# Optimization experiments

Hardware: AMD Instinct MI355X
Metric: run time of the kernel (lower is better)

Reference implementation:

```python
import jax, jax.numpy as jnp
import numpy as np

D_IN, H1, H2, B, K = 128, 128, 64, 262144, 4

def _mk(key, shape):
    return jax.random.normal(key, shape, dtype=jnp.float32) * 0.05

def setup_inputs() -> dict:
    key = jax.random.key(0)
    ks = jax.random.split(key, 40)
    inp = {
        'x': jax.random.normal(ks[0], (B, 96), dtype=jnp.float32),
        'u': jax.random.normal(ks[1], (B, 32), dtype=jnp.float32),
        'mix_factor': jax.random.uniform(ks[2], (1,), dtype=jnp.float32),
        'teacher_P': jax.random.uniform(ks[3], (K,), dtype=jnp.float32),
    }
    # main critic params (torch Linear: W [out,in], b [out])
    dims = [(H1, D_IN), (H1, H1), (H2, H1), (1, H2)] * 2  # l1..l4, l5..l8
    for i, (o, ii) in enumerate(dims):
        inp[f'W{i+1}'] = _mk(ks[4 + 2 * i], (o, ii))
        inp[f'b{i+1}'] = _mk(ks[5 + 2 * i], (o,))
    # stacked teacher params (K teachers), only l1,l2,l3,l5,l6,l7 are used
    tdims = {'1': (H1, D_IN), '2': (H1, H1), '3': (H2, H1), '5': (H1, D_IN), '6': (H1, H1), '7': (H2, H1)}
    j = 20
    for name, (o, ii) in tdims.items():
        inp[f'tW{name}'] = _mk(ks[j], (K, o, ii)); j += 1
        inp[f'tb{name}'] = _mk(ks[j], (K, o)); j += 1
    return inp

def reference(x, u, mix_factor, teacher_P, W1, b1, W2, b2, W3, b3, W4, b4, W5, b5, W6, b6, W7, b7, W8, b8, tW1, tb1, tW2, tb2, tW3, tb3, tW5, tb5, tW6, tb6, tW7, tb7):
    m = mix_factor  # [1], broadcasts
    P = teacher_P   # [K]
    xu = jnp.concatenate([x, u], axis=1)  # [B, 128]

    lin = lambda h, W, b: h @ W.T + b
    # teacher linear on shared input [B,I] -> [K,B,O]
    tlin0 = lambda h, W, b: jnp.einsum('bi,koi->kbo', h, W) + b[:, None, :]
    # teacher linear on per-teacher streams [K,B,I] -> [K,B,O]
    tlin = lambda h, W, b: jnp.einsum('kbi,koi->kbo', h, W) + b[:, None, :]
    mixsum = lambda ht: jnp.einsum('kbo,k->bo', ht, P)

    def head(W_a, b_a, W_b, b_b, W_c, b_c, W_d, b_d, tWa, tba, tWb, tbb, tWc, tbc):
        ht = tlin0(xu, tWa, tba)                                   # [K,B,128]
        h = jax.nn.relu(lin(xu, W_a, b_a) * (1 - m) + mixsum(ht) * m)
        ht = jax.nn.relu(ht)
        ht2 = tlin(ht, tWb, tbb)
        h = jax.nn.relu(lin(h, W_b, b_b) * (1 - m) + mixsum(ht2) * m)
        ht2 = jax.nn.relu(ht2)
        ht3 = tlin(ht2, tWc, tbc)
        h = jax.nn.relu(lin(h, W_c, b_c) * (1 - m) + mixsum(ht3) * m)
        return lin(h, W_d, b_d)                                    # [B,1]

    x1 = head(W1, b1, W2, b2, W3, b3, W4, b4, tW1, tb1, tW2, tb2, tW3, tb3)
    x2 = head(W5, b5, W6, b6, W7, b7, W8, b8, tW5, tb5, tW6, tb6, tW7, tb7)
    return (x1, x2)
```

## Files before the change

### kernel.cpp

```cpp
#include <hip/hip_runtime.h>
#include <hip/hip_bf16.h>
#include <stdint.h>

#define B_TOTAL 262144
#define TB 64
#define SLOT 16384
#define BUF1 81920
#define LDS_BYTES 163840
#define HEAD_W 204800

typedef short v8s __attribute__((ext_vector_type(8)));
typedef float v4f __attribute__((ext_vector_type(4)));

union Frag { uint4 q; uint32_t d[4]; v8s v; };

__device__ __forceinline__ uint32_t pack2(float a, float b) {
    union { __hip_bfloat162 h; uint32_t u; } p;
    p.h = __float22bfloat162_rn(make_float2(a, b));
    return p.u;
}


struct KParams {
    const float* x; const float* u; const float* mix; const float* P;
    const float* mb[6];
    const float* tb[6];
    const float* Wout[2];
    const float* bout[2];
    const unsigned short* wbf;
    float* out;
};

struct PrepParams { const float* src[12]; unsigned short* dst; };

__global__ __launch_bounds__(256) void prep_kernel(PrepParams pp) {
    const int ends[12] = {16384,81920,98304,163840,172032,204800,
                          221184,286720,303104,368640,376832,409600};
    int gi = (blockIdx.x * 256 + threadIdx.x) * 4;
    if (gi >= 409600) return;
    int s = 0;
    #pragma unroll
    for (int i = 0; i < 12; ++i) { if (gi >= ends[i]) s = i + 1; }
    int base = (s == 0) ? 0 : ends[s - 1];
    const float4 f = *(const float4*)(pp.src[s] + (gi - base));
    *(uint2*)(pp.dst + gi) = make_uint2(pack2(f.x, f.y), pack2(f.z, f.w));
}

__device__ __forceinline__ void stage_xu(char* lds, const float* x, const float* u,
                                         int rowBase, int tid)
{
    for (int G = tid; G < 1024; G += 512) {
        const int row = G >> 4;
        const int gg  = G & 15;
        const int grow = rowBase + row;
        float4 fa, fb;
        if (gg < 12) {
            const float* s2 = x + grow * 96 + gg * 8;
            fa = *(const float4*)s2; fb = *(const float4*)(s2 + 4);
        } else {
            const float* s2 = u + grow * 32 + (gg - 12) * 8;
            fa = *(const float4*)s2; fb = *(const float4*)(s2 + 4);
        }
        *(uint4*)(lds + row * 256 + ((gg ^ (row & 15)) << 4)) =
            make_uint4(pack2(fa.x, fa.y), pack2(fa.z, fa.w),
                       pack2(fb.x, fb.y), pack2(fb.z, fb.w));
    }
}

template<bool SHARED_IN, int N>
__device__ __forceinline__ void layer_fwd(char* lds, int inOff, int outOff,
        const unsigned short* W, const float* mbias, const float* tbias,
        float c0, const float* cP, int lane, int wave,
        const float* Wout, float* pgrid)
{
    constexpr bool FINAL = (N == 64);
    constexpr int NBT = FINAL ? 2 : 4;
    const int l15  = lane & 15;
    const int quad = lane >> 4;
    const int colBase = FINAL ? ((wave >> 1) << 4) : (wave << 4);
    const int btBase  = FINAL ? ((wave & 1) << 1) : 0;

    v4f acc[5][NBT];
    #pragma unroll
    for (int s = 0; s < 5; ++s)
        #pragma unroll
        for (int bt = 0; bt < NBT; ++bt)
            acc[s][bt] = (v4f){0.f, 0.f, 0.f, 0.f};

    const unsigned short* wRow = W + (colBase + l15) * 128 + quad * 8;

    #pragma unroll
    for (int ks = 0; ks < 4; ++ks) {
        Frag xS[NBT];
        const int gg = ks * 4 + quad;
        if constexpr (SHARED_IN) {
            #pragma unroll
            for (int bt = 0; bt < NBT; ++bt) {
                const int row = (btBase + bt) * 16 + l15;
                xS[bt].q = *(const uint4*)(lds + inOff + row * 256 + ((gg ^ (row & 15)) << 4));
            }
        }
        #pragma unroll
        for (int s = 0; s < 5; ++s) {
            Frag xF[NBT];
            if constexpr (!SHARED_IN) {
                #pragma unroll
                for (int bt = 0; bt < NBT; ++bt) {
                    const int row = (btBase + bt) * 16 + l15;
                    xF[bt].q = *(const uint4*)(lds + inOff + s * SLOT + row * 256
                                               + ((gg ^ (row & 15)) << 4));
                }
            }
            Frag wF;
            wF.q = *(const uint4*)(wRow + s * (N * 128) + ks * 32);
            #pragma unroll
            for (int bt = 0; bt < NBT; ++bt)
                acc[s][bt] = __builtin_amdgcn_mfma_f32_16x16x32_bf16(
                    wF.v, (SHARED_IN ? xS[bt].v : xF[bt].v), acc[s][bt], 0, 0, 0);
        }
    }

    const int obase = colBase + quad * 4;
    const float4 mB = *(const float4*)(mbias + obase);
    float4 tB[4];
    #pragma unroll
    for (int s = 0; s < 4; ++s)
        tB[s] = *(const float4*)(tbias + s * N + obase);

    if constexpr (!FINAL) {
        #pragma unroll
        for (int bt = 0; bt < 4; ++bt) {
            const int row = bt * 16 + l15;
            char* ab = lds + outOff + row * 256 + (((obase >> 3) ^ (row & 15)) << 4)
                       + ((obase & 7) << 1);
            float vr[4];
            vr[0] = c0 * (acc[0][bt][0] + mB.x);
            vr[1] = c0 * (acc[0][bt][1] + mB.y);
            vr[2] = c0 * (acc[0][bt][2] + mB.z);
            vr[3] = c0 * (acc[0][bt][3] + mB.w);
            uint2 tw[4];
            #pragma unroll
            for (int s = 0; s < 4; ++s) {
                float t0 = acc[s + 1][bt][0] + tB[s].x;
                float t1 = acc[s + 1][bt][1] + tB[s].y;
                float t2 = acc[s + 1][bt][2] + tB[s].z;
                float t3 = acc[s + 1][bt][3] + tB[s].w;
                vr[0] = fmaf(cP[s], t0, vr[0]);
                vr[1] = fmaf(cP[s], t1, vr[1]);
                vr[2] = fmaf(cP[s], t2, vr[2]);
                vr[3] = fmaf(cP[s], t3, vr[3]);
                tw[s] = make_uint2(pack2(fmaxf(t0, 0.f), fmaxf(t1, 0.f)),
                                   pack2(fmaxf(t2, 0.f), fmaxf(t3, 0.f)));
            }
            *(uint2*)ab = make_uint2(pack2(fmaxf(vr[0], 0.f), fmaxf(vr[1], 0.f)),
                                     pack2(fmaxf(vr[2], 0.f), fmaxf(vr[3], 0.f)));
            #pragma unroll
            for (int s = 0; s < 4; ++s)
                *(uint2*)(ab + (s + 1) * SLOT) = tw[s];
        }
    } else {
        const float4 wo = *(const float4*)(Wout + obase);
        float psum[NBT];
        #pragma unroll
        for (int j = 0; j < NBT; ++j) {
            float vr[4];
            vr[0] = c0 * (acc[0][j][0] + mB.x);
            vr[1] = c0 * (acc[0][j][1] + mB.y);
            vr[2] = c0 * (acc[0][j][2] + mB.z);
            vr[3] = c0 * (acc[0][j][3] + mB.w);
            #pragma unroll
            for (int s = 0; s < 4; ++s) {
                vr[0] = fmaf(cP[s], acc[s + 1][j][0] + tB[s].x, vr[0]);
                vr[1] = fmaf(cP[s], acc[s + 1][j][1] + tB[s].y, vr[1]);
                vr[2] = fmaf(cP[s], acc[s + 1][j][2] + tB[s].z, vr[2]);
                vr[3] = fmaf(cP[s], acc[s + 1][j][3] + tB[s].w, vr[3]);
            }
            float pp = fmaxf(vr[0], 0.f) * wo.x + fmaxf(vr[1], 0.f) * wo.y
                     + fmaxf(vr[2], 0.f) * wo.z + fmaxf(vr[3], 0.f) * wo.w;
            pp += __shfl_xor(pp, 16);
            pp += __shfl_xor(pp, 32);
            psum[j] = pp;
        }
        if (lane < 16) {
            #pragma unroll
            for (int j = 0; j < NBT; ++j)
                pgrid[(wave >> 1) * 64 + (btBase + j) * 16 + lane] = psum[j];
        }
    }
}

extern "C" __global__ __launch_bounds__(512, 2)
void critic_kernel(KParams p)
{
    extern __shared__ char lds[];
    const int tid  = threadIdx.x;
    const int lane = tid & 63;
    const int wave = tid >> 6;
    const int rowBase = blockIdx.x * TB;

    const float m  = p.mix[0];
    const float c0 = 1.f - m;
    float cP[4];
    #pragma unroll
    for (int k = 0; k < 4; ++k) cP[k] = m * p.P[k];

    stage_xu(lds, p.x, p.u, rowBase, tid);

    #pragma unroll 1
    for (int head = 0; head < 2; ++head) {
        __syncthreads();
        const unsigned short* wb = p.wbf + head * HEAD_W;
        const int hb = head * 3;

        layer_fwd<true, 128>(lds, 0, BUF1, wb, p.mb[hb + 0], p.tb[hb + 0],
                             c0, cP, lane, wave, nullptr, nullptr);
        __syncthreads();
        layer_fwd<false, 128>(lds, BUF1, 0, wb + 81920, p.mb[hb + 1], p.tb[hb + 1],
                              c0, cP, lane, wave, nullptr, nullptr);
        __syncthreads();
        layer_fwd<false, 64>(lds, 0, 0, wb + 163840, p.mb[hb + 2], p.tb[hb + 2],
                             c0, cP, lane, wave, p.Wout[head], (float*)(lds + BUF1));
        __syncthreads();

        if (tid < 64) {
            const float* pg = (const float*)(lds + BUF1);
            p.out[head * B_TOTAL + rowBase + tid] =
                p.bout[head][0] + pg[tid] + pg[64 + tid] + pg[128 + tid] + pg[192 + tid];
        }
        if (head == 0)
            stage_xu(lds, p.x, p.u, rowBase, tid);
    }
}

extern "C" void kernel_launch(void* const* d_in, const int* in_sizes, int n_in,
                              void* d_out, int out_size, void* d_ws, size_t ws_size,
                              hipStream_t stream)
{
    (void)in_sizes; (void)n_in; (void)out_size; (void)ws_size;

    PrepParams pp;
    const int sidx[12] = {4, 20, 6, 22, 8, 24, 12, 26, 14, 28, 16, 30};
    for (int i = 0; i < 12; ++i) pp.src[i] = (const float*)d_in[sidx[i]];
    pp.dst = (unsigned short*)d_ws;

    KParams kp;
    kp.x = (const float*)d_in[0];  kp.u = (const float*)d_in[1];
    kp.mix = (const float*)d_in[2]; kp.P = (const float*)d_in[3];
    const int mbi[6] = {5, 7, 9, 13, 15, 17};
    const int tbi[6] = {21, 23, 25, 27, 29, 31};
    for (int i = 0; i < 6; ++i) {
        kp.mb[i] = (const float*)d_in[mbi[i]];
        kp.tb[i] = (const float*)d_in[tbi[i]];
    }
    kp.Wout[0] = (const float*)d_in[10]; kp.Wout[1] = (const float*)d_in[18];
    kp.bout[0] = (const float*)d_in[11]; kp.bout[1] = (const float*)d_in[19];
    kp.wbf = (const unsigned short*)d_ws;
    kp.out = (float*)d_out;

    (void)hipFuncSetAttribute((const void*)critic_kernel,
                              hipFuncAttributeMaxDynamicSharedMemorySize, LDS_BYTES);

    hipLaunchKernelGGL(prep_kernel, dim3(400), dim3(256), 0, stream, pp);
    hipLaunchKernelGGL(critic_kernel, dim3(4096), dim3(512), LDS_BYTES, stream, kp);
}
```

Baseline: 883.2 us.

## Halve batch tile, raise occupancy, and prefetch double-buffered weight fragments

```diff
diff --git a/kernel.cpp b/kernel.cpp
--- a/kernel.cpp
+++ b/kernel.cpp
@@ -3,10 +3,10 @@
 #include <stdint.h>
 
 #define B_TOTAL 262144
-#define TB 64
-#define SLOT 16384
-#define BUF1 81920
-#define LDS_BYTES 163840
+#define TB 32
+#define SLOT 8192
+#define BUF1 40960
+#define LDS_BYTES 81920
 #define HEAD_W 204800
 
 typedef short v8s __attribute__((ext_vector_type(8)));
@@ -49,36 +49,52 @@
 __device__ __forceinline__ void stage_xu(char* lds, const float* x, const float* u,
                                          int rowBase, int tid)
 {
-    for (int G = tid; G < 1024; G += 512) {
-        const int row = G >> 4;
-        const int gg  = G & 15;
-        const int grow = rowBase + row;
-        float4 fa, fb;
-        if (gg < 12) {
-            const float* s2 = x + grow * 96 + gg * 8;
-            fa = *(const float4*)s2; fb = *(const float4*)(s2 + 4);
-        } else {
-            const float* s2 = u + grow * 32 + (gg - 12) * 8;
-            fa = *(const float4*)s2; fb = *(const float4*)(s2 + 4);
-        }
-        *(uint4*)(lds + row * 256 + ((gg ^ (row & 15)) << 4)) =
-            make_uint4(pack2(fa.x, fa.y), pack2(fa.z, fa.w),
-                       pack2(fb.x, fb.y), pack2(fb.z, fb.w));
-    }
+    const int row = tid >> 4;
+    const int gg  = tid & 15;
+    const int grow = rowBase + row;
+    float4 fa, fb;
+    if (gg < 12) {
+        const float* s2 = x + grow * 96 + gg * 8;
+        fa = *(const float4*)s2; fb = *(const float4*)(s2 + 4);
+    } else {
+        const float* s2 = u + grow * 32 + (gg - 12) * 8;
+        fa = *(const float4*)s2; fb = *(const float4*)(s2 + 4);
+    }
+    *(uint4*)(lds + row * 256 + ((gg ^ (row & 15)) << 4)) =
+        make_uint4(pack2(fa.x, fa.y), pack2(fa.z, fa.w),
+                   pack2(fb.x, fb.y), pack2(fb.z, fb.w));
+}
+
+struct WPre0 { Frag w0[4]; };
+
+template<int N>
+__device__ __forceinline__ WPre0 preload0(const unsigned short* W, int lane, int wave)
+{
+    WPre0 r;
+    const int l15  = lane & 15;
+    const int quad = lane >> 4;
+    const int colBase = (N == 64) ? ((wave >> 1) << 4) : (wave << 4);
+    const unsigned short* wRow = W + (colBase + l15) * 128 + quad * 8;
+    #pragma unroll
+    for (int ks = 0; ks < 4; ++ks)
+        r.w0[ks].q = *(const uint4*)(wRow + ks * 32);
+    return r;
 }
 
 template<bool SHARED_IN, int N>
-__device__ __forceinline__ void layer_fwd(char* lds, int inOff, int outOff,
-        const unsigned short* W, const float* mbias, const float* tbias,
+__device__ __forceinline__ void compute(char* lds, int inOff, int outOff,
+        const WPre0& wp, const unsigned short* W,
+        const float* mbias, const float* tbias,
         float c0, const float* cP, int lane, int wave,
         const float* Wout, float* pgrid)
 {
     constexpr bool FINAL = (N == 64);
-    constexpr int NBT = FINAL ? 2 : 4;
+    constexpr int NBT = FINAL ? 1 : 2;
     const int l15  = lane & 15;
     const int quad = lane >> 4;
     const int colBase = FINAL ? ((wave >> 1) << 4) : (wave << 4);
-    const int btBase  = FINAL ? ((wave & 1) << 1) : 0;
+    const int btBase  = FINAL ? (wave & 1) : 0;
+    const unsigned short* wRow = W + (colBase + l15) * 128 + quad * 8;
 
     v4f acc[5][NBT];
     #pragma unroll
@@ -87,36 +103,50 @@
         for (int bt = 0; bt < NBT; ++bt)
             acc[s][bt] = (v4f){0.f, 0.f, 0.f, 0.f};
 
-    const unsigned short* wRow = W + (colBase + l15) * 128 + quad * 8;
-
-    #pragma unroll
-    for (int ks = 0; ks < 4; ++ks) {
-        Frag xS[NBT];
-        const int gg = ks * 4 + quad;
-        if constexpr (SHARED_IN) {
+    Frag wf[2][4];
+    #pragma unroll
+    for (int ks = 0; ks < 4; ++ks) wf[0][ks] = wp.w0[ks];
+
+    Frag xS[4 * NBT];
+    if constexpr (SHARED_IN) {
+        #pragma unroll
+        for (int ks = 0; ks < 4; ++ks) {
+            const int gg = ks * 4 + quad;
             #pragma unroll
             for (int bt = 0; bt < NBT; ++bt) {
                 const int row = (btBase + bt) * 16 + l15;
-                xS[bt].q = *(const uint4*)(lds + inOff + row * 256 + ((gg ^ (row & 15)) << 4));
+                xS[ks * NBT + bt].q =
+                    *(const uint4*)(lds + inOff + row * 256 + ((gg ^ (row & 15)) << 4));
             }
         }
-        #pragma unroll
-        for (int s = 0; s < 5; ++s) {
-            Frag xF[NBT];
+    }
+
+    #pragma unroll
+    for (int s = 0; s < 5; ++s) {
+        if (s < 4) {
+            #pragma unroll
+            for (int ks = 0; ks < 4; ++ks)
+                wf[(s + 1) & 1][ks].q =
+                    *(const uint4*)(wRow + (s + 1) * (N * 128) + ks * 32);
+        }
+        #pragma unroll
+        for (int ks = 0; ks < 4; ++ks) {
+            const int gg = ks * 4 + quad;
+            Frag xf[NBT];
             if constexpr (!SHARED_IN) {
                 #pragma unroll
                 for (int bt = 0; bt < NBT; ++bt) {
                     const int row = (btBase + bt) * 16 + l15;
-                    xF[bt].q = *(const uint4*)(lds + inOff + s * SLOT + row * 256
+                    xf[bt].q = *(const uint4*)(lds + inOff + s * SLOT + row * 256
                                                + ((gg ^ (row & 15)) << 4));
                 }
             }
-            Frag wF;
-            wF.q = *(const uint4*)(wRow + s * (N * 128) + ks * 32);
             #pragma unroll
             for (int bt = 0; bt < NBT; ++bt)
                 acc[s][bt] = __builtin_amdgcn_mfma_f32_16x16x32_bf16(
-                    wF.v, (SHARED_IN ? xS[bt].v : xF[bt].v), acc[s][bt], 0, 0, 0);
+                    wf[s & 1][ks].v,
+                    (SHARED_IN ? xS[ks * NBT + bt].v : xf[bt].v),
+                    acc[s][bt], 0, 0, 0);
         }
     }
 
@@ -129,8 +159,8 @@
 
     if constexpr (!FINAL) {
         #pragma unroll
-        for (int bt = 0; bt < 4; ++bt) {
-            const int row = bt * 16 + l15;
+        for (int bt = 0; bt < NBT; ++bt) {
+            const int row = (btBase + bt) * 16 + l15;
             char* ab = lds + outOff + row * 256 + (((obase >> 3) ^ (row & 15)) << 4)
                        + ((obase & 7) << 1);
             float vr[4];
@@ -160,36 +190,28 @@
         }
     } else {
         const float4 wo = *(const float4*)(Wout + obase);
-        float psum[NBT];
-        #pragma unroll
-        for (int j = 0; j < NBT; ++j) {
-            float vr[4];
-            vr[0] = c0 * (acc[0][j][0] + mB.x);
-            vr[1] = c0 * (acc[0][j][1] + mB.y);
-            vr[2] = c0 * (acc[0][j][2] + mB.z);
-            vr[3] = c0 * (acc[0][j][3] + mB.w);
-            #pragma unroll
-            for (int s = 0; s < 4; ++s) {
-                vr[0] = fmaf(cP[s], acc[s + 1][j][0] + tB[s].x, vr[0]);
-                vr[1] = fmaf(cP[s], acc[s + 1][j][1] + tB[s].y, vr[1]);
-                vr[2] = fmaf(cP[s], acc[s + 1][j][2] + tB[s].z, vr[2]);
-                vr[3] = fmaf(cP[s], acc[s + 1][j][3] + tB[s].w, vr[3]);
-            }
-            float pp = fmaxf(vr[0], 0.f) * wo.x + fmaxf(vr[1], 0.f) * wo.y
-                     + fmaxf(vr[2], 0.f) * wo.z + fmaxf(vr[3], 0.f) * wo.w;
-            pp += __shfl_xor(pp, 16);
-            pp += __shfl_xor(pp, 32);
-            psum[j] = pp;
-        }
-        if (lane < 16) {
-            #pragma unroll
-            for (int j = 0; j < NBT; ++j)
-                pgrid[(wave >> 1) * 64 + (btBase + j) * 16 + lane] = psum[j];
-        }
-    }
-}
-
-extern "C" __global__ __launch_bounds__(512, 2)
+        float vr[4];
+        vr[0] = c0 * (acc[0][0][0] + mB.x);
+        vr[1] = c0 * (acc[0][0][1] + mB.y);
+        vr[2] = c0 * (acc[0][0][2] + mB.z);
+        vr[3] = c0 * (acc[0][0][3] + mB.w);
+        #pragma unroll
+        for (int s = 0; s < 4; ++s) {
+            vr[0] = fmaf(cP[s], acc[s + 1][0][0] + tB[s].x, vr[0]);
+            vr[1] = fmaf(cP[s], acc[s + 1][0][1] + tB[s].y, vr[1]);
+            vr[2] = fmaf(cP[s], acc[s + 1][0][2] + tB[s].z, vr[2]);
+            vr[3] = fmaf(cP[s], acc[s + 1][0][3] + tB[s].w, vr[3]);
+        }
+        float pp = fmaxf(vr[0], 0.f) * wo.x + fmaxf(vr[1], 0.f) * wo.y
+                 + fmaxf(vr[2], 0.f) * wo.z + fmaxf(vr[3], 0.f) * wo.w;
+        pp += __shfl_xor(pp, 16);
+        pp += __shfl_xor(pp, 32);
+        if (lane < 16)
+            pgrid[(wave >> 1) * 32 + btBase * 16 + lane] = pp;
+    }
+}
+
+extern "C" __global__ __launch_bounds__(512, 4)
 void critic_kernel(KParams p)
 {
     extern __shared__ char lds[];
@@ -208,24 +230,29 @@
 
     #pragma unroll 1
     for (int head = 0; head < 2; ++head) {
-        __syncthreads();
         const unsigned short* wb = p.wbf + head * HEAD_W;
         const int hb = head * 3;
 
-        layer_fwd<true, 128>(lds, 0, BUF1, wb, p.mb[hb + 0], p.tb[hb + 0],
-                             c0, cP, lane, wave, nullptr, nullptr);
-        __syncthreads();
-        layer_fwd<false, 128>(lds, BUF1, 0, wb + 81920, p.mb[hb + 1], p.tb[hb + 1],
-                              c0, cP, lane, wave, nullptr, nullptr);
-        __syncthreads();
-        layer_fwd<false, 64>(lds, 0, 0, wb + 163840, p.mb[hb + 2], p.tb[hb + 2],
-                             c0, cP, lane, wave, p.Wout[head], (float*)(lds + BUF1));
-        __syncthreads();
-
-        if (tid < 64) {
+        WPre0 w1 = preload0<128>(wb, lane, wave);
+        __syncthreads();
+        compute<true, 128>(lds, 0, BUF1, w1, wb, p.mb[hb + 0], p.tb[hb + 0],
+                           c0, cP, lane, wave, nullptr, nullptr);
+
+        WPre0 w2 = preload0<128>(wb + 81920, lane, wave);
+        __syncthreads();
+        compute<false, 128>(lds, BUF1, 0, w2, wb + 81920, p.mb[hb + 1], p.tb[hb + 1],
+                            c0, cP, lane, wave, nullptr, nullptr);
+
+        WPre0 w3 = preload0<64>(wb + 163840, lane, wave);
+        __syncthreads();
+        compute<false, 64>(lds, 0, 0, w3, wb + 163840, p.mb[hb + 2], p.tb[hb + 2],
+                           c0, cP, lane, wave, p.Wout[head], (float*)(lds + BUF1));
+        __syncthreads();
+
+        if (tid < TB) {
             const float* pg = (const float*)(lds + BUF1);
             p.out[head * B_TOTAL + rowBase + tid] =
-                p.bout[head][0] + pg[tid] + pg[64 + tid] + pg[128 + tid] + pg[192 + tid];
+                p.bout[head][0] + pg[tid] + pg[32 + tid] + pg[64 + tid] + pg[96 + tid];
         }
         if (head == 0)
             stage_xu(lds, p.x, p.u, rowBase, tid);
@@ -261,5 +288,5 @@
                               hipFuncAttributeMaxDynamicSharedMemorySize, LDS_BYTES);
 
     hipLaunchKernelGGL(prep_kernel, dim3(400), dim3(256), 0, stream, pp);
-    hipLaunchKernelGGL(critic_kernel, dim3(4096), dim3(512), LDS_BYTES, stream, kp);
-}
+    hipLaunchKernelGGL(critic_kernel, dim3(8192), dim3(512), LDS_BYTES, stream, kp);
+}
```

New measurement: 1.144 ms. 29.5% more time.
